# Kernel optimization log

Measured on AMD Instinct MI355X. Metric: run time of the kernel, lower is better.

## Reference

```python
import jax, jax.numpy as jnp
import numpy as np

B, S, L, H, DH, D = 16, 512, 12, 12, 64, 768
M = L + 1  # embed + L mlp outputs


def setup_inputs() -> dict:
    key = jax.random.key(0)
    ks = jax.random.split(key, 8)
    return {
        "mlp_stack": jax.random.normal(ks[0], (B, S, M, D), jnp.float32),
        "attn_stack": jax.random.normal(ks[1], (B, S, L, H, DH), jnp.float32),
        "mlp_mask": jax.random.uniform(ks[2], (B, M), jnp.float32),
        "attn_mask": jax.random.uniform(ks[3], (B, L, H), jnp.float32),
        "modal_mlp": jax.random.normal(ks[4], (M, D), jnp.float32),
        "modal_attention": jax.random.normal(ks[5], (L, H, D), jnp.float32),
        "W_O": jax.random.normal(ks[6], (L, H, DH, D), jnp.float32) * 0.02,
        "post_bias": jax.random.normal(ks[7], (L, D), jnp.float32) * 0.02,
    }


def reference(mlp_stack, attn_stack, mlp_mask, attn_mask, modal_mlp,
              modal_attention, W_O, post_bias):
    # pruning_edge_mlp_hook_all_tokens at layer_no = n_layers (final hook path),
    # cache_compressed_attn=True, ablation_backward=False, non-parallel inference.
    # masked edge-weighted sum over cached mlp outputs: [B,1,M,1]*[B,S,M,D] -> sum over M
    out = jnp.einsum('bm,bsmd->bsd', mlp_mask, mlp_stack)
    # ablation (modal) term for pruned mlp edges: broadcasts over pos
    out = out + jnp.einsum('bm,md->bd', 1.0 - mlp_mask, modal_mlp)[:, None, :]
    # masked attention-head edges, recombined through W_O:
    # ([B,1,P,H,1]*[B,S,P,H,K]) einsum [P,H,K,D] -> [B,S,D]
    attn_term = jnp.einsum('bph,bsphk,phkd->bsd', attn_mask, attn_stack, W_O)
    out = out + attn_term + post_bias.sum(axis=0)
    # ablation (modal) term for pruned attention edges, summed over layer & head
    out = out + jnp.einsum('bph,phd->bd', 1.0 - attn_mask, modal_attention)[:, None, :]
    return out
```

## Files before the change

kernel.cpp:

```cpp
#include <hip/hip_runtime.h>


#define D_ 768
#define K_ 9216
#define ROWS_ 8192
#define SPLITS 4
#define KSPLIT (K_ / SPLITS)

typedef __attribute__((ext_vector_type(8))) short short8;
typedef __attribute__((ext_vector_type(8))) unsigned short ushort8;
typedef __attribute__((ext_vector_type(4))) float f32x4;

typedef unsigned int __attribute__((address_space(1))) gu32;
typedef unsigned int __attribute__((address_space(3))) lu32;

__device__ __forceinline__ void async_copy16(const void* g, void* l) {
    __builtin_amdgcn_global_load_lds((const gu32*)g, (lu32*)l, 16, 0, 0);
}

__device__ __forceinline__ unsigned short f2bf(float f) {
    union { float f; unsigned u; } a; a.f = f;
    unsigned r = a.u + 0x7FFF + ((a.u >> 16) & 1);
    return (unsigned short)(r >> 16);
}

__global__ __launch_bounds__(256) void bias_kernel(
    const float* __restrict__ mlp_mask, const float* __restrict__ attn_mask,
    const float* __restrict__ modal_mlp, const float* __restrict__ modal_att,
    const float* __restrict__ post_bias, float* __restrict__ bias) {
    int b = blockIdx.x;
    int d = blockIdx.y * 256 + threadIdx.x;
    float acc = 0.f;
    #pragma unroll
    for (int p = 0; p < 12; ++p) acc += post_bias[p * D_ + d];
    #pragma unroll
    for (int m = 0; m < 13; ++m)
        acc += (1.f - mlp_mask[b * 13 + m]) * modal_mlp[m * D_ + d];
    #pragma unroll 16
    for (int ph = 0; ph < 144; ++ph)
        acc += (1.f - attn_mask[b * 144 + ph]) * modal_att[ph * D_ + d];
    bias[b * D_ + d] = acc;
}

__global__ __launch_bounds__(256) void transpose_wo(
    const float* __restrict__ W, unsigned short* __restrict__ Bt) {
    __shared__ float tile[32][33];
    int n0 = blockIdx.x * 32;
    int k0 = blockIdx.y * 32;
    int tx = threadIdx.x & 31, ty = threadIdx.x >> 5;
    #pragma unroll
    for (int i = 0; i < 4; ++i)
        tile[ty + 8 * i][tx] = W[(k0 + ty + 8 * i) * D_ + n0 + tx];
    __syncthreads();
    #pragma unroll
    for (int i = 0; i < 4; ++i)
        Bt[(n0 + ty + 8 * i) * K_ + k0 + tx] = f2bf(tile[tx][ty + 8 * i]);
}

__global__ __launch_bounds__(256) void conv_attn(
    const float* __restrict__ attn_stack, const float* __restrict__ attn_mask,
    unsigned short* __restrict__ A) {
    int i = (blockIdx.x * 256 + threadIdx.x) * 8;
    int row = i / K_;
    int k = i - row * K_;
    int b = row >> 9;
    float w = attn_mask[b * 144 + (k >> 6)];
    float4 v0 = *(const float4*)&attn_stack[i];
    float4 v1 = *(const float4*)&attn_stack[i + 4];
    ushort8 o;
    o[0] = f2bf(v0.x * w); o[1] = f2bf(v0.y * w);
    o[2] = f2bf(v0.z * w); o[3] = f2bf(v0.w * w);
    o[4] = f2bf(v1.x * w); o[5] = f2bf(v1.y * w);
    o[6] = f2bf(v1.z * w); o[7] = f2bf(v1.w * w);
    *(ushort8*)&A[i] = o;
}

__global__ __launch_bounds__(256) void mlp_kernel(
    const float* __restrict__ mlp_stack, const float* __restrict__ mlp_mask,
    const float* __restrict__ bias, float* __restrict__ out) {
    int i4 = (blockIdx.x * 256 + threadIdx.x) * 4;
    int row = i4 / D_;
    int d = i4 - row * D_;
    int b = row >> 9;
    float4 acc = *(const float4*)&bias[b * D_ + d];
    const float* base = mlp_stack + (long)row * 13 * D_ + d;
    #pragma unroll
    for (int m = 0; m < 13; ++m) {
        float w = mlp_mask[b * 13 + m];
        float4 v = *(const float4*)&base[m * D_];
        acc.x += w * v.x; acc.y += w * v.y;
        acc.z += w * v.z; acc.w += w * v.w;
    }
    *(float4*)&out[i4] = acc;
}

__global__ __launch_bounds__(256) void gemm_attn(
    const short* __restrict__ A, const short* __restrict__ Bt,
    float* __restrict__ out) {
    __shared__ __align__(16) short As[128 * 32];
    __shared__ __align__(16) short Bs[128 * 32];

    const int tid = threadIdx.x;
    const int wave = tid >> 6, lane = tid & 63;
    const int row0 = blockIdx.x * 128;
    const int col0 = blockIdx.y * 128;
    const int kStart = blockIdx.z * KSPLIT;
    const int wr = (wave >> 1) * 64;
    const int wc = (wave & 1) * 64;

    f32x4 acc[4][4] = {};

    const int rc = lane >> 2;
    const int x = lane & 3;
    const int g = x ^ ((rc >> 1) & 3);

    int a_off[2], b_off[2], lds_off[2];
    #pragma unroll
    for (int j = 0; j < 2; ++j) {
        int c = wave * 2 + j;
        a_off[j] = (row0 + c * 16 + rc) * K_ + g * 8 + kStart;
        b_off[j] = (col0 + c * 16 + rc) * K_ + g * 8 + kStart;
        lds_off[j] = c * 1024;
    }

    const int fr = lane & 15;
    const int q = lane >> 4;
    const int pos = q ^ ((fr >> 1) & 3);

    for (int k0 = 0; k0 < KSPLIT; k0 += 32) {
        __syncthreads();
        #pragma unroll
        for (int j = 0; j < 2; ++j) {
            async_copy16(A + a_off[j] + k0, (char*)As + lds_off[j]);
            async_copy16(Bt + b_off[j] + k0, (char*)Bs + lds_off[j]);
        }
        __syncthreads();

        short8 af[4], bf[4];
        #pragma unroll
        for (int i = 0; i < 4; ++i) {
            af[i] = *(const short8*)&As[(wr + i * 16 + fr) * 32 + pos * 8];
            bf[i] = *(const short8*)&Bs[(wc + i * 16 + fr) * 32 + pos * 8];
        }
        #pragma unroll
        for (int i = 0; i < 4; ++i)
            #pragma unroll
            for (int j = 0; j < 4; ++j)
                acc[i][j] = __builtin_amdgcn_mfma_f32_16x16x32_bf16(
                    af[i], bf[j], acc[i][j], 0, 0, 0);
    }

    #pragma unroll
    for (int i = 0; i < 4; ++i) {
        int m = row0 + wr + i * 16 + q * 4;
        #pragma unroll
        for (int j = 0; j < 4; ++j) {
            int n = col0 + wc + j * 16 + fr;
            float* p = out + m * D_ + n;
            #pragma unroll
            for (int r = 0; r < 4; ++r)
                atomicAdd(p + r * D_, acc[i][j][r]);
        }
    }
}

extern "C" void kernel_launch(void* const* d_in, const int* in_sizes, int n_in,
                              void* d_out, int out_size, void* d_ws, size_t ws_size,
                              hipStream_t stream) {
    const float* mlp_stack  = (const float*)d_in[0];
    const float* attn_stack = (const float*)d_in[1];
    const float* mlp_mask   = (const float*)d_in[2];
    const float* attn_mask  = (const float*)d_in[3];
    const float* modal_mlp  = (const float*)d_in[4];
    const float* modal_att  = (const float*)d_in[5];
    const float* W_O        = (const float*)d_in[6];
    const float* post_bias  = (const float*)d_in[7];
    float* out = (float*)d_out;

    char* ws = (char*)d_ws;
    unsigned short* Abf = (unsigned short*)ws;
    unsigned short* Btb = (unsigned short*)(ws + 150994944);
    float* bias = (float*)(ws + 150994944 + 14155776);

    bias_kernel<<<dim3(16, 3), 256, 0, stream>>>(mlp_mask, attn_mask, modal_mlp,
                                                 modal_att, post_bias, bias);
    transpose_wo<<<dim3(24, 288), 256, 0, stream>>>(W_O, Btb);
    conv_attn<<<36864, 256, 0, stream>>>(attn_stack, attn_mask, Abf);
    mlp_kernel<<<6144, 256, 0, stream>>>(mlp_stack, mlp_mask, bias, out);
    gemm_attn<<<dim3(64, 6, SPLITS), 256, 0, stream>>>((const short*)Abf,
                                                       (const short*)Btb, out);
}
```

Measured before the change: 891.9 us.

## Enlarge GEMM tile to 256x256 with double-buffered LDS and XCD-aware block remap

The attention GEMM now uses 512-thread blocks computing 256x256 output tiles, so each wave holds 4x8 MFMA accumulators. LDS is double-buffered so the next K-slice's async copies overlap the current slice's MFMAs. Split-K goes from 4 to 8, and the flat block index is remapped so that blocks sharing a K-split land on the same XCD. The aim is more data reuse per load and less load latency in the inner loop. In exchange, each output element gets twice as many atomic adds, and register and LDS pressure are higher (64KB LDS per block).

```diff
diff --git a/kernel.cpp b/kernel.cpp
--- a/kernel.cpp
+++ b/kernel.cpp
@@ -4,8 +4,10 @@
 #define D_ 768
 #define K_ 9216
 #define ROWS_ 8192
-#define SPLITS 4
+#define SPLITS 8
 #define KSPLIT (K_ / SPLITS)
+#define BK 32
+#define NT (KSPLIT / BK)
 
 typedef __attribute__((ext_vector_type(8))) short short8;
 typedef __attribute__((ext_vector_type(8))) unsigned short ushort8;
@@ -94,67 +96,85 @@
     *(float4*)&out[i4] = acc;
 }
 
-__global__ __launch_bounds__(256) void gemm_attn(
+__global__ __launch_bounds__(512, 2) void gemm_attn(
     const short* __restrict__ A, const short* __restrict__ Bt,
     float* __restrict__ out) {
-    __shared__ __align__(16) short As[128 * 32];
-    __shared__ __align__(16) short Bs[128 * 32];
+    __shared__ __align__(16) short As[2][256 * 32];
+    __shared__ __align__(16) short Bs[2][256 * 32];
+
+    const int bid = (int)blockIdx.x;
+    const int l = (bid & 7) * 96 + (bid >> 3);
+    const int z = l / 96;
+    const int rem = l - z * 96;
+    const int ytile = rem >> 5;
+    const int xtile = rem & 31;
 
     const int tid = threadIdx.x;
     const int wave = tid >> 6, lane = tid & 63;
-    const int row0 = blockIdx.x * 128;
-    const int col0 = blockIdx.y * 128;
-    const int kStart = blockIdx.z * KSPLIT;
+    const int row0 = xtile * 256;
+    const int col0 = ytile * 256;
+    const int kStart = z * KSPLIT;
     const int wr = (wave >> 1) * 64;
-    const int wc = (wave & 1) * 64;
-
-    f32x4 acc[4][4] = {};
+    const int wc = (wave & 1) * 128;
+
+    f32x4 acc[4][8] = {};
 
     const int rc = lane >> 2;
     const int x = lane & 3;
     const int g = x ^ ((rc >> 1) & 3);
 
-    int a_off[2], b_off[2], lds_off[2];
+    int a_off[2], b_off[2], lof[2];
     #pragma unroll
     for (int j = 0; j < 2; ++j) {
         int c = wave * 2 + j;
         a_off[j] = (row0 + c * 16 + rc) * K_ + g * 8 + kStart;
         b_off[j] = (col0 + c * 16 + rc) * K_ + g * 8 + kStart;
-        lds_off[j] = c * 1024;
+        lof[j] = c * 1024;
     }
 
     const int fr = lane & 15;
     const int q = lane >> 4;
     const int pos = q ^ ((fr >> 1) & 3);
 
-    for (int k0 = 0; k0 < KSPLIT; k0 += 32) {
-        __syncthreads();
-        #pragma unroll
-        for (int j = 0; j < 2; ++j) {
-            async_copy16(A + a_off[j] + k0, (char*)As + lds_off[j]);
-            async_copy16(Bt + b_off[j] + k0, (char*)Bs + lds_off[j]);
+    #pragma unroll
+    for (int j = 0; j < 2; ++j) {
+        async_copy16(A + a_off[j], (char*)As[0] + lof[j]);
+        async_copy16(Bt + b_off[j], (char*)Bs[0] + lof[j]);
+    }
+    __syncthreads();
+
+    int cur = 0;
+    for (int t = 0; t < NT; ++t) {
+        if (t + 1 < NT) {
+            const int k0 = (t + 1) * BK;
+            #pragma unroll
+            for (int j = 0; j < 2; ++j) {
+                async_copy16(A + a_off[j] + k0, (char*)As[cur ^ 1] + lof[j]);
+                async_copy16(Bt + b_off[j] + k0, (char*)Bs[cur ^ 1] + lof[j]);
+            }
         }
-        __syncthreads();
-
-        short8 af[4], bf[4];
-        #pragma unroll
-        for (int i = 0; i < 4; ++i) {
-            af[i] = *(const short8*)&As[(wr + i * 16 + fr) * 32 + pos * 8];
-            bf[i] = *(const short8*)&Bs[(wc + i * 16 + fr) * 32 + pos * 8];
-        }
+        short8 af[4], bf[8];
+        #pragma unroll
+        for (int i = 0; i < 4; ++i)
+            af[i] = *(const short8*)&As[cur][(wr + i * 16 + fr) * 32 + pos * 8];
+        #pragma unroll
+        for (int j = 0; j < 8; ++j)
+            bf[j] = *(const short8*)&Bs[cur][(wc + j * 16 + fr) * 32 + pos * 8];
         #pragma unroll
         for (int i = 0; i < 4; ++i)
             #pragma unroll
-            for (int j = 0; j < 4; ++j)
+            for (int j = 0; j < 8; ++j)
                 acc[i][j] = __builtin_amdgcn_mfma_f32_16x16x32_bf16(
                     af[i], bf[j], acc[i][j], 0, 0, 0);
+        __syncthreads();
+        cur ^= 1;
     }
 
     #pragma unroll
     for (int i = 0; i < 4; ++i) {
         int m = row0 + wr + i * 16 + q * 4;
         #pragma unroll
-        for (int j = 0; j < 4; ++j) {
+        for (int j = 0; j < 8; ++j) {
             int n = col0 + wc + j * 16 + fr;
             float* p = out + m * D_ + n;
             #pragma unroll
@@ -187,6 +207,5 @@
     transpose_wo<<<dim3(24, 288), 256, 0, stream>>>(W_O, Btb);
     conv_attn<<<36864, 256, 0, stream>>>(attn_stack, attn_mask, Abf);
     mlp_kernel<<<6144, 256, 0, stream>>>(mlp_stack, mlp_mask, bias, out);
-    gemm_attn<<<dim3(64, 6, SPLITS), 256, 0, stream>>>((const short*)Abf,
-                                                       (const short*)Btb, out);
-}
+    gemm_attn<<<768, 512, 0, stream>>>((const short*)Abf, (const short*)Btb, out);
+}
```

After: 969.7 us. 1.09x slower.
